# Performance work log

Measured on AMD Instinct MI355X. Metric: run time of the kernel, lower is better.

## Reference

```python
import jax, jax.numpy as jnp
import numpy as np

B, N, C = 2, 2048, 2048
H, KV = 16, 4          # query heads, kv heads
D = C // H             # head_dim = 128
ROPE_BASE = 10000.0


def rope_cos_sin(position_ids, dim):
    # interleaved RoPE: freqs for even indices, repeated pairwise to full dim
    inv_freq = 1.0 / (ROPE_BASE ** (jnp.arange(0, dim, 2, dtype=jnp.float32) / dim))
    ang = position_ids[..., None].astype(jnp.float32) * inv_freq   # [B, N, D/2]
    cos = jnp.repeat(jnp.cos(ang), 2, axis=-1)                     # [B, N, D]
    sin = jnp.repeat(jnp.sin(ang), 2, axis=-1)
    return cos, sin


def rotate_half_interleaved(x):
    # (x0, x1, x2, x3, ...) -> (-x1, x0, -x3, x2, ...)
    x1 = x[..., 0::2]
    x2 = x[..., 1::2]
    return jnp.stack([-x2, x1], axis=-1).reshape(x.shape)


def apply_rotary(x, cos, sin):
    # x: [B, h, N, D]; cos/sin: [B, N, D]
    return x * cos[:, None] + rotate_half_interleaved(x) * sin[:, None]


def setup_inputs() -> dict:
    key = jax.random.key(0)
    ks = jax.random.split(key, 5)
    s = 0.02
    return dict(
        x=jax.random.normal(ks[0], (B, N, C), jnp.float32),
        position_ids=jnp.tile(jnp.arange(N, dtype=jnp.int32), (B, 1)),
        Wq=jax.random.normal(ks[1], (C, C), jnp.float32) * s,
        bq=jnp.zeros((C,), jnp.float32),
        Wk=jax.random.normal(ks[2], (C, KV * D), jnp.float32) * s,
        bk=jnp.zeros((KV * D,), jnp.float32),
        Wv=jax.random.normal(ks[3], (C, KV * D), jnp.float32) * s,
        bv=jnp.zeros((KV * D,), jnp.float32),
        Wo=jax.random.normal(ks[4], (C, C), jnp.float32) * s,
    )


def reference(x, position_ids, Wq, bq, Wk, bk, Wv, bv, Wo):
    Bx, Nx, Cx = x.shape
    q = (x @ Wq + bq).reshape(Bx, Nx, H, D).transpose(0, 2, 1, 3)   # [B,H,N,D]
    k = (x @ Wk + bk).reshape(Bx, Nx, KV, D).transpose(0, 2, 1, 3)  # [B,KV,N,D]
    v = (x @ Wv + bv).reshape(Bx, Nx, KV, D).transpose(0, 2, 1, 3)

    cos, sin = rope_cos_sin(position_ids, D)
    q = apply_rotary(q, cos, sin)
    k = apply_rotary(k, cos, sin)

    # GQA expand: head h uses kv head h // groups (matches unsqueeze+expand+reshape)
    groups = H // KV
    k = jnp.repeat(k, groups, axis=1)   # [B,H,N,D]
    v = jnp.repeat(v, groups, axis=1)

    attn = jnp.einsum('bhqd,bhkd->bhqk', q, k) * (D ** -0.5)        # [B,H,N,N]
    causal_mask = jnp.triu(jnp.ones((Nx, Nx), dtype=bool), 1)
    attn = jnp.where(causal_mask, -jnp.inf, attn)
    attn = jax.nn.softmax(attn, axis=-1)

    out = jnp.einsum('bhqk,bhkd->bhqd', attn, v)
    out = out.transpose(0, 2, 1, 3).reshape(Bx, Nx, Cx)
    return out @ Wo
```

## Files before the change

kernel.cpp:

```cpp
#include <hip/hip_runtime.h>
#include <cstdint>

typedef unsigned short u16;
typedef unsigned int u32;
typedef __bf16 bf16x8 __attribute__((ext_vector_type(8)));
typedef short s16x8 __attribute__((ext_vector_type(8)));
typedef float f32x4 __attribute__((ext_vector_type(4)));

constexpr int BB = 2;
constexpr int SEQ = 2048;
constexpr int CH = 2048;
constexpr int NH = 16;
constexpr int NKV = 4;
constexpr int HD = 128;
constexpr int QKVC = CH + 2 * NKV * HD;

#define DI __device__ __forceinline__

DI u16 f2b(float x) {
  u32 u = __float_as_uint(x);
  u = u + 0x7FFFu + ((u >> 16) & 1u);
  return (u16)(u >> 16);
}
DI float b2f(u16 u) { return __uint_as_float(((u32)u) << 16); }

DI void glds16(const void* g, void* l) {
  __builtin_amdgcn_global_load_lds(
      (__attribute__((address_space(1))) void*)(uintptr_t)g,
      (__attribute__((address_space(3))) void*)(u32)(uintptr_t)l, 16, 0, 0);
}

__global__ __launch_bounds__(256) void xconv_kernel(const float* __restrict__ in,
                                                    u16* __restrict__ out, int n4) {
  int i = blockIdx.x * 256 + threadIdx.x;
  if (i < n4) {
    float4 v = *(const float4*)&in[(size_t)i * 4];
    ushort4 o;
    o.x = f2b(v.x); o.y = f2b(v.y); o.z = f2b(v.z); o.w = f2b(v.w);
    *(ushort4*)&out[(size_t)i * 4] = o;
  }
}

__global__ __launch_bounds__(256) void wtrans_kernel(const float* __restrict__ in,
                                                     u16* __restrict__ out,
                                                     int R, int Cc, int ostride) {
  __shared__ u16 tile[64 * 65];
  const int r0 = blockIdx.x * 64, c0 = blockIdx.y * 64;
  const int tid = threadIdx.x;
  for (int c = tid; c < 1024; c += 256) {
    int r = c >> 4, col = (c & 15) * 4;
    float4 v = *(const float4*)&in[(size_t)(r0 + r) * Cc + c0 + col];
    tile[r * 65 + col + 0] = f2b(v.x);
    tile[r * 65 + col + 1] = f2b(v.y);
    tile[r * 65 + col + 2] = f2b(v.z);
    tile[r * 65 + col + 3] = f2b(v.w);
  }
  __syncthreads();
  for (int c = tid; c < 1024; c += 256) {
    int r = c >> 4, col = (c & 15) * 4;
    ushort4 v;
    v.x = tile[(col + 0) * 65 + r];
    v.y = tile[(col + 1) * 65 + r];
    v.z = tile[(col + 2) * 65 + r];
    v.w = tile[(col + 3) * 65 + r];
    *(ushort4*)&out[(size_t)(c0 + r) * ostride + r0 + col] = v;
  }
}

__global__ __launch_bounds__(256) void vtrans_kernel(const u16* __restrict__ in,
                                                     u16* __restrict__ out) {
  __shared__ u16 tile[64 * 65];
  const int s = blockIdx.z, n0 = blockIdx.x * 64, d0 = blockIdx.y * 64;
  const int tid = threadIdx.x;
  const u16* ip = in + (size_t)s * SEQ * HD + (size_t)n0 * HD + d0;
  u16* op = out + (size_t)s * HD * SEQ + (size_t)d0 * SEQ + n0;
  for (int c = tid; c < 1024; c += 256) {
    int r = c >> 4, col = (c & 15) * 4;
    ushort4 v = *(const ushort4*)&ip[(size_t)r * HD + col];
    tile[r * 65 + col + 0] = v.x;
    tile[r * 65 + col + 1] = v.y;
    tile[r * 65 + col + 2] = v.z;
    tile[r * 65 + col + 3] = v.w;
  }
  __syncthreads();
  for (int c = tid; c < 1024; c += 256) {
    int r = c >> 4, col = (c & 15) * 4;
    ushort4 v;
    v.x = tile[(col + 0) * 65 + r];
    v.y = tile[(col + 1) * 65 + r];
    v.z = tile[(col + 2) * 65 + r];
    v.w = tile[(col + 3) * 65 + r];
    int u = col;
    int w = (u & 3) | (((u >> 5) & 1) << 2) | (((u >> 2) & 3) << 3) | (((u >> 4) & 1) << 5);
    int glp = (w >> 3) ^ (r & 7);
    int colp = glp * 8 + (w & 7);
    *(ushort4*)&op[(size_t)r * SEQ + colp] = v;
  }
}

template <int MODE>
__global__ __launch_bounds__(256, 2) void gemm_kernel(
    const u16* __restrict__ A, const u16* __restrict__ Bt,
    u16* __restrict__ Cb, float* __restrict__ Cf,
    const float* __restrict__ bq, const float* __restrict__ bk,
    const float* __restrict__ bv, int M, int Nn, int K) {
  __shared__ u16 As[128 * 32];
  __shared__ u16 Bs[128 * 32];
  const int tid = threadIdx.x;
  const int lane = tid & 63, wave = tid >> 6;
  const int wrow = wave >> 1, wcol = wave & 1;
  const int m0 = blockIdx.x * 128, n0 = blockIdx.y * 128;
  const int lm = lane & 15, lq = lane >> 4;
  f32x4 acc[4][4] = {};

  const u16* ag = A + (size_t)(m0 + (tid >> 2)) * K + (tid & 3) * 8;
  const u16* bg = Bt + (size_t)(n0 + (tid >> 2)) * K + (tid & 3) * 8;
  char* asb = (char*)As + wave * 1024;
  char* bsb = (char*)Bs + wave * 1024;
  const size_t rowskip = (size_t)64 * K;

  for (int k = 0; k < K; k += 32) {
    __syncthreads();
    glds16(ag + k, asb);
    glds16(ag + rowskip + k, asb + 4096);
    glds16(bg + k, bsb);
    glds16(bg + rowskip + k, bsb + 4096);
    __syncthreads();
    bf16x8 af[4], bfr[4];
#pragma unroll
    for (int i = 0; i < 4; i++)
      af[i] = *(const bf16x8*)&As[(wrow * 64 + i * 16 + lm) * 32 + lq * 8];
#pragma unroll
    for (int j = 0; j < 4; j++)
      bfr[j] = *(const bf16x8*)&Bs[(wcol * 64 + j * 16 + lm) * 32 + lq * 8];
#pragma unroll
    for (int i = 0; i < 4; i++)
#pragma unroll
      for (int j = 0; j < 4; j++)
        acc[i][j] = __builtin_amdgcn_mfma_f32_16x16x32_bf16(af[i], bfr[j], acc[i][j], 0, 0, 0);
  }

#pragma unroll
  for (int i = 0; i < 4; i++) {
    const int mg = m0 + wrow * 64 + i * 16 + lq * 4;
#pragma unroll
    for (int j = 0; j < 4; j++) {
      const int ng = n0 + wcol * 64 + j * 16 + lm;
      float bias = 0.f;
      if (MODE == 0)
        bias = (ng < CH) ? bq[ng] : (ng < CH + NKV * HD ? bk[ng - CH] : bv[ng - CH - NKV * HD]);
#pragma unroll
      for (int r = 0; r < 4; r++) {
        float v = acc[i][j][r] + bias;
        size_t off = (size_t)(mg + r) * Nn + ng;
        if (MODE == 0) Cb[off] = f2b(v);
        else           Cf[off] = v;
      }
    }
  }
}

__global__ __launch_bounds__(256) void rope_kernel(
    const u16* __restrict__ qkv, const int* __restrict__ pos,
    u16* __restrict__ Qo, u16* __restrict__ Ko, u16* __restrict__ Vn) {
  const int tok = blockIdx.x;
  const int b = tok >> 11, n = tok & (SEQ - 1);
  const int t = threadIdx.x;
  const float p = (float)pos[tok];
  const u16* row = qkv + (size_t)tok * QKVC;
  const float LN1E4_64 = 0.14391156831212788f;

  for (int idx = t; idx < NH * 64; idx += 256) {
    int hh = idx >> 6, i = idx & 63;
    float ang = p * expf(-(float)i * LN1E4_64);
    float sn, cs;
    sincosf(ang, &sn, &cs);
    float q0v = b2f(row[hh * 128 + 2 * i]);
    float q1v = b2f(row[hh * 128 + 2 * i + 1]);
    size_t off = ((size_t)(b * NH + hh) * SEQ + n) * HD + 2 * i;
    Qo[off] = f2b(q0v * cs - q1v * sn);
    Qo[off + 1] = f2b(q1v * cs + q0v * sn);
  }
  {
    int kh = t >> 6, i = t & 63;
    float ang = p * expf(-(float)i * LN1E4_64);
    float sn, cs;
    sincosf(ang, &sn, &cs);
    float k0v = b2f(row[CH + kh * 128 + 2 * i]);
    float k1v = b2f(row[CH + kh * 128 + 2 * i + 1]);
    int d0 = 2 * i;
    int g = d0 >> 3;
    int gp = (g & 8) | ((g ^ n) & 7);
    int dp = gp * 8 + (d0 & 7);
    size_t off = ((size_t)(b * NKV + kh) * SEQ + n) * HD + dp;
    Ko[off] = f2b(k0v * cs - k1v * sn);
    Ko[off + 1] = f2b(k1v * cs + k0v * sn);
  }
  for (int idx = t; idx < NKV * HD; idx += 256) {
    int kh = idx >> 7, d = idx & 127;
    Vn[((size_t)(b * NKV + kh) * SEQ + n) * HD + d] = row[CH + NKV * HD + kh * 128 + d];
  }
}

__global__ __launch_bounds__(256, 2) void flash_kernel(
    const u16* __restrict__ Q, const u16* __restrict__ Kk,
    const u16* __restrict__ Vt, u16* __restrict__ Oo) {
  __shared__ u16 Kb[2][64 * 128];
  __shared__ u16 Vb[2][128 * 64];
  const int tid = threadIdx.x, lane = tid & 63, wave = tid >> 6;
  const int lm = lane & 15, lq = lane >> 4;
  const int qb = gridDim.x - 1 - blockIdx.x;
  const int h = blockIdx.y, b = blockIdx.z;
  const int q0 = qb * 128;
  const int kvh = h >> 2;
  const u16* Qg = Q + ((size_t)(b * NH + h) * SEQ + q0) * HD;
  const u16* Kg = Kk + (size_t)(b * NKV + kvh) * SEQ * HD;
  const u16* Vg = Vt + (size_t)(b * NKV + kvh) * HD * SEQ;

  bf16x8 qf[2][4];
#pragma unroll
  for (int qg = 0; qg < 2; qg++) {
    const u16* qrow = Qg + (size_t)(wave * 32 + qg * 16 + lm) * HD;
#pragma unroll
    for (int kd = 0; kd < 4; kd++)
      qf[qg][kd] = *(const bf16x8*)&qrow[kd * 32 + lq * 8];
  }

  f32x4 oacc[2][8] = {};
  float rs[2] = {0.f, 0.f};
  const float SCL2 = 0.12754325f;
  const int nIter = 2 * qb + 2;

  auto stage = [&](int kv0, int bufi) {
    const char* kb = (const char*)(Kg + (size_t)kv0 * HD);
    char* kl = (char*)&Kb[bufi][0];
    const char* vbb = (const char*)(Vg + (size_t)kv0);
    char* vl = (char*)&Vb[bufi][0];
#pragma unroll
    for (int c = 0; c < 4; c++) {
      int ch = wave * 4 + c;
      glds16(kb + ch * 1024 + lane * 16, kl + ch * 1024);
      glds16(vbb + (size_t)(ch * 8 + (lane >> 3)) * (SEQ * 2) + (lane & 7) * 16,
             vl + ch * 1024);
    }
  };

  stage(0, 0);

  for (int t = 0; t < nIter; t++) {
    __syncthreads();
    if (t + 1 < nIter) stage((t + 1) * 64, (t + 1) & 1);
    const u16* Ks = &Kb[t & 1][0];
    const u16* Vs = &Vb[t & 1][0];
    const int kv0 = t * 64;
    if (kv0 > q0 + wave * 32 + 31) continue;

    f32x4 sv[2][4] = {};
    const int gp = ((lq & 8) ) | ((lq ^ lm) & 7);
#pragma unroll
    for (int nt = 0; nt < 4; nt++) {
#pragma unroll
      for (int kd = 0; kd < 4; kd++) {
        int g = kd * 4 + lq;
        int gpp = (g & 8) | ((g ^ lm) & 7);
        bf16x8 kf = *(const bf16x8*)&Ks[(nt * 16 + lm) * 128 + gpp * 8];
        sv[0][nt] = __builtin_amdgcn_mfma_f32_16x16x32_bf16(kf, qf[0][kd], sv[0][nt], 0, 0, 0);
        sv[1][nt] = __builtin_amdgcn_mfma_f32_16x16x32_bf16(kf, qf[1][kd], sv[1][nt], 0, 0, 0);
      }
    }
    (void)gp;

    s16x8 pa[2][2];
#pragma unroll
    for (int qg = 0; qg < 2; qg++) {
      const int base = q0 + wave * 32 + qg * 16;
      if (kv0 + 63 > base) {
        const int qrow = base + lm;
#pragma unroll
        for (int nt = 0; nt < 4; nt++)
#pragma unroll
          for (int r = 0; r < 4; r++) {
            int kvg = kv0 + nt * 16 + lq * 4 + r;
            float p = exp2f(sv[qg][nt][r] * SCL2);
            if (kvg > qrow) p = 0.f;
            rs[qg] += p;
            pa[qg][nt & 1][(nt >> 1) * 4 + r] = (short)f2b(p);
          }
      } else {
#pragma unroll
        for (int nt = 0; nt < 4; nt++)
#pragma unroll
          for (int r = 0; r < 4; r++) {
            float p = exp2f(sv[qg][nt][r] * SCL2);
            rs[qg] += p;
            pa[qg][nt & 1][(nt >> 1) * 4 + r] = (short)f2b(p);
          }
      }
    }

#pragma unroll
    for (int ks = 0; ks < 2; ks++) {
      const int glp = (ks * 4 + lq) ^ (lm & 7);
#pragma unroll
      for (int dt = 0; dt < 8; dt++) {
        bf16x8 vf = *(const bf16x8*)&Vs[(dt * 16 + lm) * 64 + glp * 8];
        oacc[0][dt] = __builtin_amdgcn_mfma_f32_16x16x32_bf16(
            *(bf16x8*)&pa[0][ks], vf, oacc[0][dt], 0, 0, 0);
        oacc[1][dt] = __builtin_amdgcn_mfma_f32_16x16x32_bf16(
            *(bf16x8*)&pa[1][ks], vf, oacc[1][dt], 0, 0, 0);
      }
    }
  }

  u16* orow = Oo + (size_t)b * SEQ * CH + (size_t)h * HD;
#pragma unroll
  for (int qg = 0; qg < 2; qg++) {
    float r0 = rs[qg];
    r0 += __shfl_xor(r0, 16);
    r0 += __shfl_xor(r0, 32);
    float inv[4];
#pragma unroll
    for (int r = 0; r < 4; r++) inv[r] = 1.0f / __shfl(r0, lq * 4 + r);
    const int qrow_base = q0 + wave * 32 + qg * 16 + lq * 4;
#pragma unroll
    for (int dt = 0; dt < 8; dt++)
#pragma unroll
      for (int r = 0; r < 4; r++)
        orow[(size_t)(qrow_base + r) * CH + dt * 16 + lm] = f2b(oacc[qg][dt][r] * inv[r]);
  }
}

extern "C" void kernel_launch(void* const* d_in, const int* in_sizes, int n_in,
                              void* d_out, int out_size, void* d_ws, size_t ws_size,
                              hipStream_t stream) {
  const float* x = (const float*)d_in[0];
  const int* pos = (const int*)d_in[1];
  const float* Wq = (const float*)d_in[2];
  const float* bq = (const float*)d_in[3];
  const float* Wk = (const float*)d_in[4];
  const float* bk = (const float*)d_in[5];
  const float* Wv = (const float*)d_in[6];
  const float* bv = (const float*)d_in[7];
  const float* Wo = (const float*)d_in[8];
  float* out = (float*)d_out;

  char* ws = (char*)d_ws;
  u16* xb = (u16*)ws;    ws += (size_t)BB * SEQ * CH * 2;
  u16* wqkvt = (u16*)ws; ws += (size_t)QKVC * CH * 2;
  u16* wot = (u16*)ws;   ws += (size_t)CH * CH * 2;
  u16* qkv = (u16*)ws;   ws += (size_t)BB * SEQ * QKVC * 2;
  u16* qr = (u16*)ws;    ws += (size_t)BB * NH * SEQ * HD * 2;
  u16* kr = (u16*)ws;    ws += (size_t)BB * NKV * SEQ * HD * 2;
  u16* vn = (u16*)ws;    ws += (size_t)BB * NKV * SEQ * HD * 2;
  u16* vt = (u16*)ws;    ws += (size_t)BB * NKV * SEQ * HD * 2;
  u16* ao = (u16*)ws;    ws += (size_t)BB * SEQ * CH * 2;

  xconv_kernel<<<dim3(BB * SEQ * CH / 1024), 256, 0, stream>>>(x, xb, BB * SEQ * CH / 4);
  wtrans_kernel<<<dim3(32, 32), 256, 0, stream>>>(Wq, wqkvt, CH, CH, CH);
  wtrans_kernel<<<dim3(32, 8), 256, 0, stream>>>(Wk, wqkvt + (size_t)CH * CH, CH, NKV * HD, CH);
  wtrans_kernel<<<dim3(32, 8), 256, 0, stream>>>(Wv, wqkvt + (size_t)(CH + NKV * HD) * CH, CH, NKV * HD, CH);
  wtrans_kernel<<<dim3(32, 32), 256, 0, stream>>>(Wo, wot, CH, CH, CH);
  gemm_kernel<0><<<dim3(32, 24), 256, 0, stream>>>(xb, wqkvt, qkv, (float*)nullptr,
                                                   bq, bk, bv, BB * SEQ, QKVC, CH);
  rope_kernel<<<dim3(BB * SEQ), 256, 0, stream>>>(qkv, pos, qr, kr, vn);
  vtrans_kernel<<<dim3(SEQ / 64, HD / 64, BB * NKV), 256, 0, stream>>>(vn, vt);
  flash_kernel<<<dim3(SEQ / 128, NH, BB), 256, 0, stream>>>(qr, kr, vt, ao);
  gemm_kernel<1><<<dim3(32, 16), 256, 0, stream>>>(ao, wot, (u16*)nullptr, out,
                                                   nullptr, nullptr, nullptr, BB * SEQ, CH, CH);
}
```

Before: 346.7 us.

## Balance causal flash blocks by pairing query tiles, merge weight transposes, share RoPE tables

```diff
diff --git a/kernel.cpp b/kernel.cpp
--- a/kernel.cpp
+++ b/kernel.cpp
@@ -1,5 +1,6 @@
 #include <hip/hip_runtime.h>
 #include <cstdint>
+#include <type_traits>
 
 typedef unsigned short u16;
 typedef unsigned int u32;
@@ -41,9 +42,20 @@
   }
 }
 
-__global__ __launch_bounds__(256) void wtrans_kernel(const float* __restrict__ in,
-                                                     u16* __restrict__ out,
-                                                     int R, int Cc, int ostride) {
+__global__ __launch_bounds__(256) void wtrans4_kernel(
+    const float* __restrict__ Wq, const float* __restrict__ Wk,
+    const float* __restrict__ Wv, const float* __restrict__ Wo,
+    u16* __restrict__ wqkvt, u16* __restrict__ wot) {
+  const int z = blockIdx.z;
+  const float* in;
+  u16* out;
+  int Cc;
+  if (z == 0)      { in = Wq; out = wqkvt;                                Cc = CH; }
+  else if (z == 1) { in = Wk; out = wqkvt + (size_t)CH * CH;              Cc = NKV * HD; }
+  else if (z == 2) { in = Wv; out = wqkvt + (size_t)(CH + NKV * HD) * CH; Cc = NKV * HD; }
+  else             { in = Wo; out = wot;                                  Cc = CH; }
+  if ((int)blockIdx.y * 64 >= Cc) return;
+
   __shared__ u16 tile[64 * 65];
   const int r0 = blockIdx.x * 64, c0 = blockIdx.y * 64;
   const int tid = threadIdx.x;
@@ -63,7 +75,7 @@
     v.y = tile[(col + 1) * 65 + r];
     v.z = tile[(col + 2) * 65 + r];
     v.w = tile[(col + 3) * 65 + r];
-    *(ushort4*)&out[(size_t)(c0 + r) * ostride + r0 + col] = v;
+    *(ushort4*)&out[(size_t)(c0 + r) * CH + r0 + col] = v;
   }
 }
 
@@ -99,7 +111,7 @@
 }
 
 template <int MODE>
-__global__ __launch_bounds__(256, 2) void gemm_kernel(
+__global__ __launch_bounds__(256, 3) void gemm_kernel(
     const u16* __restrict__ A, const u16* __restrict__ Bt,
     u16* __restrict__ Cb, float* __restrict__ Cf,
     const float* __restrict__ bq, const float* __restrict__ bk,
@@ -163,18 +175,25 @@
 __global__ __launch_bounds__(256) void rope_kernel(
     const u16* __restrict__ qkv, const int* __restrict__ pos,
     u16* __restrict__ Qo, u16* __restrict__ Ko, u16* __restrict__ Vn) {
+  __shared__ float cs_s[64], sn_s[64];
   const int tok = blockIdx.x;
   const int b = tok >> 11, n = tok & (SEQ - 1);
   const int t = threadIdx.x;
-  const float p = (float)pos[tok];
   const u16* row = qkv + (size_t)tok * QKVC;
   const float LN1E4_64 = 0.14391156831212788f;
 
+  if (t < 64) {
+    float ang = (float)pos[tok] * expf(-(float)t * LN1E4_64);
+    float sn, cs;
+    sincosf(ang, &sn, &cs);
+    cs_s[t] = cs;
+    sn_s[t] = sn;
+  }
+  __syncthreads();
+
   for (int idx = t; idx < NH * 64; idx += 256) {
     int hh = idx >> 6, i = idx & 63;
-    float ang = p * expf(-(float)i * LN1E4_64);
-    float sn, cs;
-    sincosf(ang, &sn, &cs);
+    float cs = cs_s[i], sn = sn_s[i];
     float q0v = b2f(row[hh * 128 + 2 * i]);
     float q1v = b2f(row[hh * 128 + 2 * i + 1]);
     size_t off = ((size_t)(b * NH + hh) * SEQ + n) * HD + 2 * i;
@@ -183,9 +202,7 @@
   }
   {
     int kh = t >> 6, i = t & 63;
-    float ang = p * expf(-(float)i * LN1E4_64);
-    float sn, cs;
-    sincosf(ang, &sn, &cs);
+    float cs = cs_s[i], sn = sn_s[i];
     float k0v = b2f(row[CH + kh * 128 + 2 * i]);
     float k1v = b2f(row[CH + kh * 128 + 2 * i + 1]);
     int d0 = 2 * i;
@@ -209,18 +226,19 @@
   __shared__ u16 Vb[2][128 * 64];
   const int tid = threadIdx.x, lane = tid & 63, wave = tid >> 6;
   const int lm = lane & 15, lq = lane >> 4;
-  const int qb = gridDim.x - 1 - blockIdx.x;
+  const int p = blockIdx.x;
   const int h = blockIdx.y, b = blockIdx.z;
-  const int q0 = qb * 128;
+  const int q0A = p * 64, q0B = (31 - p) * 64;
   const int kvh = h >> 2;
-  const u16* Qg = Q + ((size_t)(b * NH + h) * SEQ + q0) * HD;
+  const u16* Qg = Q + (size_t)(b * NH + h) * SEQ * HD;
   const u16* Kg = Kk + (size_t)(b * NKV + kvh) * SEQ * HD;
   const u16* Vg = Vt + (size_t)(b * NKV + kvh) * HD * SEQ;
 
   bf16x8 qf[2][4];
 #pragma unroll
   for (int qg = 0; qg < 2; qg++) {
-    const u16* qrow = Qg + (size_t)(wave * 32 + qg * 16 + lm) * HD;
+    const int q0g = qg ? q0B : q0A;
+    const u16* qrow = Qg + (size_t)(q0g + wave * 16 + lm) * HD;
 #pragma unroll
     for (int kd = 0; kd < 4; kd++)
       qf[qg][kd] = *(const bf16x8*)&qrow[kd * 32 + lq * 8];
@@ -229,7 +247,7 @@
   f32x4 oacc[2][8] = {};
   float rs[2] = {0.f, 0.f};
   const float SCL2 = 0.12754325f;
-  const int nIter = 2 * qb + 2;
+  const int nIter = 32 - p;
 
   auto stage = [&](int kv0, int bufi) {
     const char* kb = (const char*)(Kg + (size_t)kv0 * HD);
@@ -253,75 +271,81 @@
     const u16* Ks = &Kb[t & 1][0];
     const u16* Vs = &Vb[t & 1][0];
     const int kv0 = t * 64;
-    if (kv0 > q0 + wave * 32 + 31) continue;
-
-    f32x4 sv[2][4] = {};
-    const int gp = ((lq & 8) ) | ((lq ^ lm) & 7);
-#pragma unroll
-    for (int nt = 0; nt < 4; nt++) {
-#pragma unroll
-      for (int kd = 0; kd < 4; kd++) {
-        int g = kd * 4 + lq;
-        int gpp = (g & 8) | ((g ^ lm) & 7);
-        bf16x8 kf = *(const bf16x8*)&Ks[(nt * 16 + lm) * 128 + gpp * 8];
-        sv[0][nt] = __builtin_amdgcn_mfma_f32_16x16x32_bf16(kf, qf[0][kd], sv[0][nt], 0, 0, 0);
-        sv[1][nt] = __builtin_amdgcn_mfma_f32_16x16x32_bf16(kf, qf[1][kd], sv[1][nt], 0, 0, 0);
+    const bool actA = (t <= p);
+
+    auto run = [&](auto dualc) {
+      constexpr bool DUAL = decltype(dualc)::value;
+      f32x4 sv[2][4] = {};
+#pragma unroll
+      for (int nt = 0; nt < 4; nt++)
+#pragma unroll
+        for (int kd = 0; kd < 4; kd++) {
+          int g = kd * 4 + lq;
+          int gpp = (g & 8) | ((g ^ lm) & 7);
+          bf16x8 kf = *(const bf16x8*)&Ks[(nt * 16 + lm) * 128 + gpp * 8];
+          sv[1][nt] = __builtin_amdgcn_mfma_f32_16x16x32_bf16(kf, qf[1][kd], sv[1][nt], 0, 0, 0);
+          if constexpr (DUAL)
+            sv[0][nt] = __builtin_amdgcn_mfma_f32_16x16x32_bf16(kf, qf[0][kd], sv[0][nt], 0, 0, 0);
+        }
+
+      s16x8 pa[2][2];
+      auto softmax = [&](int qg, int q0g) {
+        const int base = q0g + wave * 16;
+        if (kv0 + 63 > base) {
+          const int qrow = base + lm;
+#pragma unroll
+          for (int nt = 0; nt < 4; nt++)
+#pragma unroll
+            for (int r = 0; r < 4; r++) {
+              int kvg = kv0 + nt * 16 + lq * 4 + r;
+              float pv = exp2f(sv[qg][nt][r] * SCL2);
+              if (kvg > qrow) pv = 0.f;
+              rs[qg] += pv;
+              pa[qg][nt & 1][(nt >> 1) * 4 + r] = (short)f2b(pv);
+            }
+        } else {
+#pragma unroll
+          for (int nt = 0; nt < 4; nt++)
+#pragma unroll
+            for (int r = 0; r < 4; r++) {
+              float pv = exp2f(sv[qg][nt][r] * SCL2);
+              rs[qg] += pv;
+              pa[qg][nt & 1][(nt >> 1) * 4 + r] = (short)f2b(pv);
+            }
+        }
+      };
+      softmax(1, q0B);
+      if constexpr (DUAL) softmax(0, q0A);
+
+#pragma unroll
+      for (int ks = 0; ks < 2; ks++) {
+        const int glp = (ks * 4 + lq) ^ (lm & 7);
+#pragma unroll
+        for (int dt = 0; dt < 8; dt++) {
+          bf16x8 vf = *(const bf16x8*)&Vs[(dt * 16 + lm) * 64 + glp * 8];
+          oacc[1][dt] = __builtin_amdgcn_mfma_f32_16x16x32_bf16(
+              *(bf16x8*)&pa[1][ks], vf, oacc[1][dt], 0, 0, 0);
+          if constexpr (DUAL)
+            oacc[0][dt] = __builtin_amdgcn_mfma_f32_16x16x32_bf16(
+                *(bf16x8*)&pa[0][ks], vf, oacc[0][dt], 0, 0, 0);
+        }
       }
-    }
-    (void)gp;
-
-    s16x8 pa[2][2];
-#pragma unroll
-    for (int qg = 0; qg < 2; qg++) {
-      const int base = q0 + wave * 32 + qg * 16;
-      if (kv0 + 63 > base) {
-        const int qrow = base + lm;
-#pragma unroll
-        for (int nt = 0; nt < 4; nt++)
-#pragma unroll
-          for (int r = 0; r < 4; r++) {
-            int kvg = kv0 + nt * 16 + lq * 4 + r;
-            float p = exp2f(sv[qg][nt][r] * SCL2);
-            if (kvg > qrow) p = 0.f;
-            rs[qg] += p;
-            pa[qg][nt & 1][(nt >> 1) * 4 + r] = (short)f2b(p);
-          }
-      } else {
-#pragma unroll
-        for (int nt = 0; nt < 4; nt++)
-#pragma unroll
-          for (int r = 0; r < 4; r++) {
-            float p = exp2f(sv[qg][nt][r] * SCL2);
-            rs[qg] += p;
-            pa[qg][nt & 1][(nt >> 1) * 4 + r] = (short)f2b(p);
-          }
-      }
-    }
-
-#pragma unroll
-    for (int ks = 0; ks < 2; ks++) {
-      const int glp = (ks * 4 + lq) ^ (lm & 7);
-#pragma unroll
-      for (int dt = 0; dt < 8; dt++) {
-        bf16x8 vf = *(const bf16x8*)&Vs[(dt * 16 + lm) * 64 + glp * 8];
-        oacc[0][dt] = __builtin_amdgcn_mfma_f32_16x16x32_bf16(
-            *(bf16x8*)&pa[0][ks], vf, oacc[0][dt], 0, 0, 0);
-        oacc[1][dt] = __builtin_amdgcn_mfma_f32_16x16x32_bf16(
-            *(bf16x8*)&pa[1][ks], vf, oacc[1][dt], 0, 0, 0);
-      }
-    }
+    };
+    if (actA) run(std::integral_constant<bool, true>{});
+    else      run(std::integral_constant<bool, false>{});
   }
 
   u16* orow = Oo + (size_t)b * SEQ * CH + (size_t)h * HD;
 #pragma unroll
   for (int qg = 0; qg < 2; qg++) {
+    const int q0g = qg ? q0B : q0A;
     float r0 = rs[qg];
     r0 += __shfl_xor(r0, 16);
     r0 += __shfl_xor(r0, 32);
     float inv[4];
 #pragma unroll
     for (int r = 0; r < 4; r++) inv[r] = 1.0f / __shfl(r0, lq * 4 + r);
-    const int qrow_base = q0 + wave * 32 + qg * 16 + lq * 4;
+    const int qrow_base = q0g + wave * 16 + lq * 4;
 #pragma unroll
     for (int dt = 0; dt < 8; dt++)
 #pragma unroll
@@ -356,15 +380,12 @@
   u16* ao = (u16*)ws;    ws += (size_t)BB * SEQ * CH * 2;
 
   xconv_kernel<<<dim3(BB * SEQ * CH / 1024), 256, 0, stream>>>(x, xb, BB * SEQ * CH / 4);
-  wtrans_kernel<<<dim3(32, 32), 256, 0, stream>>>(Wq, wqkvt, CH, CH, CH);
-  wtrans_kernel<<<dim3(32, 8), 256, 0, stream>>>(Wk, wqkvt + (size_t)CH * CH, CH, NKV * HD, CH);
-  wtrans_kernel<<<dim3(32, 8), 256, 0, stream>>>(Wv, wqkvt + (size_t)(CH + NKV * HD) * CH, CH, NKV * HD, CH);
-  wtrans_kernel<<<dim3(32, 32), 256, 0, stream>>>(Wo, wot, CH, CH, CH);
+  wtrans4_kernel<<<dim3(32, 32, 4), 256, 0, stream>>>(Wq, Wk, Wv, Wo, wqkvt, wot);
   gemm_kernel<0><<<dim3(32, 24), 256, 0, stream>>>(xb, wqkvt, qkv, (float*)nullptr,
                                                    bq, bk, bv, BB * SEQ, QKVC, CH);
   rope_kernel<<<dim3(BB * SEQ), 256, 0, stream>>>(qkv, pos, qr, kr, vn);
   vtrans_kernel<<<dim3(SEQ / 64, HD / 64, BB * NKV), 256, 0, stream>>>(vn, vt);
-  flash_kernel<<<dim3(SEQ / 128, NH, BB), 256, 0, stream>>>(qr, kr, vt, ao);
+  flash_kernel<<<dim3(16, NH, BB), 256, 0, stream>>>(qr, kr, vt, ao);
   gemm_kernel<1><<<dim3(32, 16), 256, 0, stream>>>(ao, wot, (u16*)nullptr, out,
                                                    nullptr, nullptr, nullptr, BB * SEQ, CH, CH);
 }
```

Result: faster. 321.4 us (-7.3%).
